# Kernel optimization log

Measured on AMD Instinct MI355X. Metric: run time of the kernel, lower is better.

## Reference

```python
import jax, jax.numpy as jnp
import numpy as np

N_CHARS = 50257
CHAR = 512
HID = 1024
LENGTH = 2048


def setup_inputs() -> dict:
    key = jax.random.key(0)
    ks = jax.random.split(key, 8)
    s = 1.0 / np.sqrt(HID)
    sh = 1.0 / np.sqrt(HID)
    return {
        "inputs": jax.random.normal(ks[0], (HID,), jnp.float32),
        "embed": (jax.random.normal(ks[1], (N_CHARS, CHAR), jnp.float32) * 0.02),
        "W_ih": jax.random.uniform(ks[2], (4 * HID, CHAR), jnp.float32, -s, s),
        "W_hh": jax.random.uniform(ks[3], (4 * HID, HID), jnp.float32, -s, s),
        "b_ih": jax.random.uniform(ks[4], (4 * HID,), jnp.float32, -s, s),
        "b_hh": jax.random.uniform(ks[5], (4 * HID,), jnp.float32, -s, s),
        "W_head": jax.random.uniform(ks[6], (N_CHARS, HID), jnp.float32, -sh, sh),
        "b_head": jax.random.uniform(ks[7], (N_CHARS,), jnp.float32, -sh, sh),
        "length": LENGTH,
        "start": 5,
    }


def _lstm_cell(x, h, c, W_ih, W_hh, b_ih, b_hh):
    # PyTorch gate order: i, f, g, o
    gates = W_ih @ x + b_ih + W_hh @ h + b_hh  # [4H]
    i, f, g, o = jnp.split(gates, 4)
    i = jax.nn.sigmoid(i)
    f = jax.nn.sigmoid(f)
    g = jnp.tanh(g)
    o = jax.nn.sigmoid(o)
    c = f * c + i * g
    h = o * jnp.tanh(c)
    return h, c


def reference(inputs, embed, W_ih, W_hh, b_ih, b_hh, W_head, b_head, length, start):
    h0 = inputs                       # latent used as initial hidden state
    c0 = jnp.zeros_like(inputs)
    x0 = embed[start]                 # [CHAR]

    def step(carry, _):
        h, c, x = carry
        h, c = _lstm_cell(x, h, c, W_ih, W_hh, b_ih, b_hh)
        logits = W_head @ h + b_head  # [N_CHARS]
        char = jnp.argmax(logits)
        x = embed[char]
        return (h, c, x), (char, logits)

    _, (chars, logits) = jax.lax.scan(step, (h0, c0, x0), None, length=length)
    return chars, logits
```

## Files before the change

kernel.cpp:

```cpp
#include <hip/hip_runtime.h>
#include <stdint.h>
#include <math.h>

#define HID   1024
#define CHARD 512
#define NC    50257
#define TLEN  2048
#define NBLK  256
#define NTHR  512
#define NGRP2 2048
#define GR    25
#define GRREG 6
#define GRLDS 19
#define NBH   1571
#define SQ    4064.0f
#define INVSQ (1.0f/4064.0f)
#define QERR  (0.5f/4064.0f)
#define CANDR 192
#define FLAGSTRIDE 16

typedef unsigned long long ull;
typedef unsigned char u8;
typedef float f32x4 __attribute__((ext_vector_type(4)));

__device__ __forceinline__ unsigned ford(float f) {
    unsigned b = __float_as_uint(f);
    return (b & 0x80000000u) ? ~b : (b | 0x80000000u);
}
__device__ __forceinline__ float unford(unsigned u) {
    return __uint_as_float((u & 0x80000000u) ? (u & 0x7FFFFFFFu) : ~u);
}
__device__ __forceinline__ ull packkv(float v, unsigned j) {
    return ((ull)ford(v) << 32) | (ull)(0xFFFFFFFFu - j);
}
__device__ __forceinline__ ull umaxu(ull a, ull b) { return a > b ? a : b; }
__device__ __forceinline__ ull shflx_ull(ull v, int m) {
    unsigned lo = (unsigned)v, hi = (unsigned)(v >> 32);
    lo = __shfl_xor(lo, m);
    hi = __shfl_xor(hi, m);
    return ((ull)hi << 32) | lo;
}

#define ALOADF(p)    __hip_atomic_load((p), __ATOMIC_RELAXED, __HIP_MEMORY_SCOPE_AGENT)
#define ASTORE(p, v) __hip_atomic_store((p), (v), __ATOMIC_RELAXED, __HIP_MEMORY_SCOPE_AGENT)

__global__ __launch_bounds__(256) void k_init(const float* __restrict__ inputs,
                                              float* __restrict__ hh,
                                              float* __restrict__ c,
                                              unsigned* __restrict__ flagarea)
{
    int g = blockIdx.x * 256 + threadIdx.x;
    if (g < HID) { hh[g] = inputs[g]; c[g] = 0.f; }
    for (int i = g; i < 2 * NBLK * FLAGSTRIDE + 16; i += 2048) flagarea[i] = 0u;
}

__global__ __launch_bounds__(256) void k_quant(const float* __restrict__ W,
                                               u8* __restrict__ W8)
{
    size_t base = ((size_t)blockIdx.x * 256 + threadIdx.x) * 16;
    if (base >= (size_t)NC * HID) return;
    const float4* src = (const float4*)(W + base);
    uint out[4];
    #pragma unroll
    for (int g = 0; g < 4; ++g) {
        float4 w = src[g];
        int a0 = (__float2int_rn(w.x * SQ) + 128) & 255;
        int a1 = (__float2int_rn(w.y * SQ) + 128) & 255;
        int a2 = (__float2int_rn(w.z * SQ) + 128) & 255;
        int a3 = (__float2int_rn(w.w * SQ) + 128) & 255;
        out[g] = (uint)(a0 | (a1 << 8) | (a2 << 16) | (a3 << 24));
    }
    *(uint4*)(W8 + base) = make_uint4(out[0], out[1], out[2], out[3]);
}

__device__ __forceinline__ float exact_logit(const float4* hs4,
                                             const float* __restrict__ W_head,
                                             const float* __restrict__ b_head,
                                             int j, int lane)
{
    const float4* wr = (const float4*)(W_head + (size_t)j * HID);
    float a = 0.f;
    #pragma unroll
    for (int m = 0; m < 4; ++m) {
        float4 w = wr[m * 64 + lane], v = hs4[m * 64 + lane];
        a = fmaf(w.x, v.x, a); a = fmaf(w.y, v.y, a);
        a = fmaf(w.z, v.z, a); a = fmaf(w.w, v.w, a);
    }
    #pragma unroll
    for (int off = 32; off > 0; off >>= 1) a += __shfl_xor(a, off);
    return a + b_head[j];
}

__device__ __forceinline__ unsigned resolve_char(const float4* hs4,
                                                 ull* bm, float* abuf,
                                                 const float* __restrict__ W_head,
                                                 const float* __restrict__ b_head,
                                                 float Sh, ull* red8, int tid)
{
    __shared__ int s_cnt, s_gcnt;
    __shared__ int s_grps[32];
    __shared__ int s_rows[CANDR];

    const int wave = tid >> 6;
    const int lane = tid & 63;

    ull bmv[4];
    ull pm = 0ull;
    #pragma unroll
    for (int rep = 0; rep < NGRP2 / NTHR; ++rep) {
        bmv[rep] = ALOADF(&bm[tid + rep * NTHR]);
        pm = umaxu(pm, bmv[rep]);
    }
    #pragma unroll
    for (int off = 32; off > 0; off >>= 1) pm = umaxu(pm, shflx_ull(pm, off));
    if (lane == 0) red8[wave] = pm;
    if (tid == 0) { s_cnt = 0; s_gcnt = 0; }
    __syncthreads();
    pm = red8[0];
    #pragma unroll
    for (int w = 1; w < 8; ++w) pm = umaxu(pm, red8[w]);
    const float mtil = unford((unsigned)(pm >> 32));
    const float E = QERR * Sh * 1.02f + 1e-4f;
    const float thresh = mtil - 2.0f * E;
    const ull pkth = ((ull)ford(thresh)) << 32;

    #pragma unroll
    for (int rep = 0; rep < NGRP2 / NTHR; ++rep) {
        if (bmv[rep] >= pkth) {
            int p = atomicAdd(&s_gcnt, 1);
            if (p < 32) s_grps[p] = tid + rep * NTHR;
        }
    }
    __syncthreads();
    const int ngr = s_gcnt;
    int ncr;
    if (ngr <= 32) {
        for (int gq = 0; gq < ngr; ++gq) {
            const int j = s_grps[gq] * GR + tid;
            if (tid < GR && j < NC) {
                float av = ALOADF(&abuf[j]);
                if (av >= thresh) {
                    int p = atomicAdd(&s_cnt, 1);
                    if (p < CANDR) s_rows[p] = j;
                }
            }
        }
        __syncthreads();
        ncr = s_cnt;
    } else {
        ncr = CANDR + 1;
    }

    ull best = 0ull;
    if (ncr <= CANDR) {
        for (int q = wave; q < ncr; q += 8) {
            const int j = s_rows[q];
            best = umaxu(best, packkv(exact_logit(hs4, W_head, b_head, j, lane),
                                      (unsigned)j));
        }
    } else {
        for (int i = wave; i < NGRP2; i += 8) {
            ull bv = ALOADF(&bm[i]);
            if (bv >= pkth) {
                const int jb = i * GR;
                const int je = jb + GR < NC ? jb + GR : NC;
                for (int j = jb; j < je; ++j) {
                    float av = ALOADF(&abuf[j]);
                    if (av >= thresh)
                        best = umaxu(best, packkv(exact_logit(hs4, W_head, b_head, j, lane),
                                                  (unsigned)j));
                }
            }
        }
    }
    __syncthreads();
    if (lane == 0) red8[wave] = best;
    __syncthreads();
    best = red8[0];
    #pragma unroll
    for (int w = 1; w < 8; ++w) best = umaxu(best, red8[w]);
    unsigned idx = 0xFFFFFFFFu - (unsigned)(best & 0xFFFFFFFFull);
    return idx < NC ? idx : (NC - 1);
}

__device__ __forceinline__ float dot16u(uint4 q, float4 h0, float4 h1,
                                        float4 h2, float4 h3)
{
    float a = 0.f;
    a = fmaf((float)(q.x & 255u), h0.x, a);
    a = fmaf((float)((q.x >> 8) & 255u), h0.y, a);
    a = fmaf((float)((q.x >> 16) & 255u), h0.z, a);
    a = fmaf((float)(q.x >> 24), h0.w, a);
    a = fmaf((float)(q.y & 255u), h1.x, a);
    a = fmaf((float)((q.y >> 8) & 255u), h1.y, a);
    a = fmaf((float)((q.y >> 16) & 255u), h1.z, a);
    a = fmaf((float)(q.y >> 24), h1.w, a);
    a = fmaf((float)(q.z & 255u), h2.x, a);
    a = fmaf((float)((q.z >> 8) & 255u), h2.y, a);
    a = fmaf((float)((q.z >> 16) & 255u), h2.z, a);
    a = fmaf((float)(q.z >> 24), h2.w, a);
    a = fmaf((float)(q.w & 255u), h3.x, a);
    a = fmaf((float)((q.w >> 8) & 255u), h3.y, a);
    a = fmaf((float)((q.w >> 16) & 255u), h3.z, a);
    a = fmaf((float)(q.w >> 24), h3.w, a);
    return a;
}

__global__ __launch_bounds__(NTHR, 1) void k_persist(
    const float* __restrict__ W_ih, const float* __restrict__ W_hh,
    const float* __restrict__ b_ih, const float* __restrict__ b_hh,
    const float* __restrict__ embed,
    const float* __restrict__ W_head, const float* __restrict__ b_head,
    const u8* __restrict__ W8,
    float* hh, float* abuf, ull* bm,
    float* __restrict__ chars_out, const int* __restrict__ startp,
    unsigned* flags, unsigned* gen)
{
    __shared__ uint4  w8L[8][GRLDS][64];
    __shared__ float4 hs4[HID / 4];
    __shared__ float4 xs4[CHARD / 4];
    __shared__ ull    red8[8];
    __shared__ float  sred[8], sred2[8];
    __shared__ int    s_brk;

    const int b    = blockIdx.x;
    const int tid  = threadIdx.x;
    const int wave = tid >> 6;
    const int lane = tid & 63;
    const int rL   = b * 4 + wave;
    const int g    = b * 8 + wave;
    const int jb   = g * GR;
    const u8* Wp   = W8 + (size_t)jb * HID;

    uint4 qb[GRREG];
    #pragma unroll
    for (int rr = 0; rr < GRREG; ++rr) {
        const int j = jb + rr;
        qb[rr] = (j < NC) ? ((const uint4*)(Wp + (size_t)rr * HID))[lane]
                          : make_uint4(0, 0, 0, 0);
    }
    #pragma unroll
    for (int rr = 0; rr < GRLDS; ++rr) {
        const int j = jb + GRREG + rr;
        w8L[wave][rr][lane] = (j < NC)
            ? ((const uint4*)(Wp + (size_t)(GRREG + rr) * HID))[lane]
            : make_uint4(0, 0, 0, 0);
    }

    float bsum[4] = {0.f, 0.f, 0.f, 0.f};
    if (wave < 4) {
        #pragma unroll
        for (int q = 0; q < 4; ++q) bsum[q] = b_ih[q * HID + rL] + b_hh[q * HID + rL];
    }
    if (tid == 0) s_brk = 0;
    float creg = 0.f;
    __syncthreads();

    float Sh;
    {
        float sa = 0.f;
        if (tid < 256) {
            float4 hv = ((const float4*)hh)[tid];
            hs4[tid] = hv;
            sa = fabsf(hv.x) + fabsf(hv.y) + fabsf(hv.z) + fabsf(hv.w);
        }
        #pragma unroll
        for (int off = 32; off > 0; off >>= 1) sa += __shfl_xor(sa, off);
        if (lane == 0) sred[wave] = sa;
        __syncthreads();
        Sh = 0.f;
        #pragma unroll
        for (int w = 0; w < 8; ++w) Sh += sred[w];
    }

    unsigned bk = 0;

    #define GRIDBAR()                                                              \
    do {                                                                           \
        ++bk;                                                                      \
        __syncthreads();                                                           \
        if (b == 0) {                                                              \
            if (!s_brk && tid > 0 && tid < NBLK) {                                 \
                int guard = 0;                                                     \
                while (__hip_atomic_load(&flags[tid * FLAGSTRIDE],                 \
                         __ATOMIC_RELAXED, __HIP_MEMORY_SCOPE_AGENT) < bk) {       \
                    __builtin_amdgcn_s_sleep(1);                                   \
                    if (++guard > (1 << 24)) { s_brk = 1; break; }                 \
                }                                                                  \
            }                                                                      \
            __syncthreads();                                                       \
            if (tid < NBLK)                                                        \
                __hip_atomic_store(&gen[tid * FLAGSTRIDE], bk, __ATOMIC_RELAXED,   \
                                   __HIP_MEMORY_SCOPE_AGENT);                      \
        } else {                                                                   \
            if (tid == 0) {                                                        \
                __hip_atomic_store(&flags[b * FLAGSTRIDE], bk, __ATOMIC_RELAXED,   \
                                   __HIP_MEMORY_SCOPE_AGENT);                      \
                if (!s_brk) {                                                      \
                    int guard = 0;                                                 \
                    while (__hip_atomic_load(&gen[b * FLAGSTRIDE],                 \
                             __ATOMIC_RELAXED, __HIP_MEMORY_SCOPE_AGENT) < bk) {   \
                        __builtin_amdgcn_s_sleep(1);                               \
                        if (++guard > (1 << 24)) { s_brk = 1; break; }             \
                    }                                                              \
                }                                                                  \
            }                                                                      \
            __syncthreads();                                                       \
        }                                                                          \
    } while (0)

    for (int t = 0; t < TLEN; ++t) {
        unsigned idx;
        if (t == 0) {
            idx = (unsigned)startp[0];
        } else {
            idx = resolve_char(hs4, bm, abuf, W_head, b_head, Sh, red8, tid);
            if (b == 0 && tid == 0) chars_out[t - 1] = (float)idx;
        }
        if (tid < 128) xs4[tid] = ((const float4*)(embed + (size_t)idx * CHARD))[tid];
        __syncthreads();

        if (wave < 4) {
            float acc[4];
            #pragma unroll
            for (int q = 0; q < 4; ++q) {
                const float4* wi = (const float4*)(W_ih + (size_t)(q * HID + rL) * CHARD);
                const float4* wh = (const float4*)(W_hh + (size_t)(q * HID + rL) * HID);
                float a = 0.f;
                #pragma unroll
                for (int m = 0; m < 2; ++m) {
                    float4 w = wi[m * 64 + lane], v = xs4[m * 64 + lane];
                    a = fmaf(w.x, v.x, a); a = fmaf(w.y, v.y, a);
                    a = fmaf(w.z, v.z, a); a = fmaf(w.w, v.w, a);
                }
                #pragma unroll
                for (int m = 0; m < 4; ++m) {
                    float4 w = wh[m * 64 + lane], v = hs4[m * 64 + lane];
                    a = fmaf(w.x, v.x, a); a = fmaf(w.y, v.y, a);
                    a = fmaf(w.z, v.z, a); a = fmaf(w.w, v.w, a);
                }
                acc[q] = a;
            }
            #pragma unroll
            for (int q = 0; q < 4; ++q) {
                #pragma unroll
                for (int off = 32; off > 0; off >>= 1) acc[q] += __shfl_xor(acc[q], off);
            }
            if (lane == 0) {
                float ig = 1.f / (1.f + expf(-(acc[0] + bsum[0])));
                float fg = 1.f / (1.f + expf(-(acc[1] + bsum[1])));
                float gg = tanhf(acc[2] + bsum[2]);
                float og = 1.f / (1.f + expf(-(acc[3] + bsum[3])));
                creg = fg * creg + ig * gg;
                ASTORE(&hh[(size_t)(t + 1) * HID + rL], og * tanhf(creg));
            }
        }

        GRIDBAR();

        {
            float sa = 0.f, ss = 0.f;
            if (tid < 256) {
                float4 hv = ((const float4*)(hh + (size_t)(t + 1) * HID))[tid];
                hs4[tid] = hv;
                sa = fabsf(hv.x) + fabsf(hv.y) + fabsf(hv.z) + fabsf(hv.w);
                ss = hv.x + hv.y + hv.z + hv.w;
            }
            #pragma unroll
            for (int off = 32; off > 0; off >>= 1) {
                sa += __shfl_xor(sa, off);
                ss += __shfl_xor(ss, off);
            }
            if (lane == 0) { sred[wave] = sa; sred2[wave] = ss; }
        }
        __syncthreads();
        float Hsum = 0.f;
        Sh = 0.f;
        #pragma unroll
        for (int w = 0; w < 8; ++w) { Sh += sred[w]; Hsum += sred2[w]; }

        const float4 H0 = hs4[lane * 4 + 0];
        const float4 H1 = hs4[lane * 4 + 1];
        const float4 H2 = hs4[lane * 4 + 2];
        const float4 H3 = hs4[lane * 4 + 3];

        ull pmw = 0ull;
        #pragma unroll
        for (int rr = 0; rr < GRREG; ++rr) {
            const int j = jb + rr;
            if (j < NC) {
                float a = dot16u(qb[rr], H0, H1, H2, H3);
                #pragma unroll
                for (int off = 32; off > 0; off >>= 1) a += __shfl_xor(a, off);
                const float v = (a - 128.f * Hsum) * INVSQ + b_head[j];
                if (lane == 0) ASTORE(&abuf[j], v);
                pmw = umaxu(pmw, packkv(v, (unsigned)j));
            }
        }
        #pragma unroll
        for (int rr = 0; rr < GRLDS; ++rr) {
            const int j = jb + GRREG + rr;
            if (j < NC) {
                float a = dot16u(w8L[wave][rr][lane], H0, H1, H2, H3);
                #pragma unroll
                for (int off = 32; off > 0; off >>= 1) a += __shfl_xor(a, off);
                const float v = (a - 128.f * Hsum) * INVSQ + b_head[j];
                if (lane == 0) ASTORE(&abuf[j], v);
                pmw = umaxu(pmw, packkv(v, (unsigned)j));
            }
        }
        if (lane == 0) ASTORE(&bm[g], pmw);

        GRIDBAR();
    }

    if (b == 0) {
        unsigned idx = resolve_char(hs4, bm, abuf, W_head, b_head, Sh, red8, tid);
        if (tid == 0) chars_out[TLEN - 1] = (float)idx;
    }
    #undef GRIDBAR
}

#define GJ 64
#define GT 128
#define GK 16
__global__ __launch_bounds__(256) void k_gemm(const float* __restrict__ W_head,
                                              const float* __restrict__ b_head,
                                              const float* __restrict__ hh,
                                              float* __restrict__ logits)
{
    __shared__ float Ws[GK][GJ + 4];
    __shared__ float Hs[GK][GT + 1];

    const int tid = threadIdx.x;
    const int j0 = blockIdx.x * GJ;
    const int t0 = blockIdx.y * GT;
    const int tj = tid & 15;
    const int tt = tid >> 4;

    const int wlj = tid >> 2;
    const int wlk = (tid & 3) * 4;
    const int hlt = tid >> 1;
    const int hlk = (tid & 1) * 8;
    const float* Wrow = W_head + (size_t)(j0 + wlj) * HID;
    const bool wvalid = (j0 + wlj) < NC;

    float acc[8][4];
    #pragma unroll
    for (int bb = 0; bb < 8; ++bb)
        #pragma unroll
        for (int a = 0; a < 4; ++a) acc[bb][a] = 0.f;

    for (int k0 = 0; k0 < HID; k0 += GK) {
        __syncthreads();
        float4 wv = wvalid ? *(const float4*)(Wrow + k0 + wlk) : make_float4(0, 0, 0, 0);
        Ws[wlk + 0][wlj] = wv.x; Ws[wlk + 1][wlj] = wv.y;
        Ws[wlk + 2][wlj] = wv.z; Ws[wlk + 3][wlj] = wv.w;
        const float* hp = hh + (size_t)(t0 + hlt + 1) * HID + k0 + hlk;
        float4 a0 = *(const float4*)hp;
        float4 a1 = *(const float4*)(hp + 4);
        Hs[hlk + 0][hlt] = a0.x; Hs[hlk + 1][hlt] = a0.y;
        Hs[hlk + 2][hlt] = a0.z; Hs[hlk + 3][hlt] = a0.w;
        Hs[hlk + 4][hlt] = a1.x; Hs[hlk + 5][hlt] = a1.y;
        Hs[hlk + 6][hlt] = a1.z; Hs[hlk + 7][hlt] = a1.w;
        __syncthreads();
        #pragma unroll
        for (int kk = 0; kk < GK; ++kk) {
            float4 w4 = *(const float4*)&Ws[kk][tj * 4];
            float hvv[8];
            #pragma unroll
            for (int bb = 0; bb < 8; ++bb) hvv[bb] = Hs[kk][tt + 16 * bb];
            #pragma unroll
            for (int bb = 0; bb < 8; ++bb) {
                acc[bb][0] = fmaf(w4.x, hvv[bb], acc[bb][0]);
                acc[bb][1] = fmaf(w4.y, hvv[bb], acc[bb][1]);
                acc[bb][2] = fmaf(w4.z, hvv[bb], acc[bb][2]);
                acc[bb][3] = fmaf(w4.w, hvv[bb], acc[bb][3]);
            }
        }
    }

    const int j = j0 + tj * 4;
    float b0 = (j + 0 < NC) ? b_head[j + 0] : 0.f;
    float b1 = (j + 1 < NC) ? b_head[j + 1] : 0.f;
    float b2 = (j + 2 < NC) ? b_head[j + 2] : 0.f;
    float b3 = (j + 3 < NC) ? b_head[j + 3] : 0.f;
    #pragma unroll
    for (int bb = 0; bb < 8; ++bb) {
        const int t = t0 + tt + 16 * bb;
        float* dst = logits + (size_t)t * NC + j;
        if (j + 3 < NC) {
            f32x4 o = { acc[bb][0] + b0, acc[bb][1] + b1,
                        acc[bb][2] + b2, acc[bb][3] + b3 };
            __builtin_nontemporal_store(o, (f32x4*)dst);
        } else {
            if (j + 0 < NC) dst[0] = acc[bb][0] + b0;
            if (j + 1 < NC) dst[1] = acc[bb][1] + b1;
            if (j + 2 < NC) dst[2] = acc[bb][2] + b2;
        }
    }
}

__global__ __launch_bounds__(256) void k_init_fb(const float* __restrict__ inputs,
                                                 const int* __restrict__ startp,
                                                 float* __restrict__ h0,
                                                 float* __restrict__ c,
                                                 ull* __restrict__ blockmax)
{
    int tid = blockIdx.x * 256 + threadIdx.x;
    if (tid < NBH) blockmax[tid] = (tid == 0) ? packkv(3.0e38f, (unsigned)startp[0]) : 0ull;
    if (tid < HID) { h0[tid] = inputs[tid]; c[tid] = 0.f; }
}

__global__ __launch_bounds__(256) void k_lstm_fb(const float* __restrict__ W_ih,
                                                 const float* __restrict__ W_hh,
                                                 const float* __restrict__ b_ih,
                                                 const float* __restrict__ b_hh,
                                                 const float* __restrict__ embed,
                                                 const ull* __restrict__ blockmax,
                                                 const float* __restrict__ h_in,
                                                 float* __restrict__ h_out,
                                                 float* __restrict__ c,
                                                 float* __restrict__ chars_out,
                                                 int t)
{
    __shared__ float4 xs4[CHARD / 4];
    __shared__ float4 hs4[HID / 4];
    __shared__ ull    red[256];
    const int tid = threadIdx.x;
    ull pm = 0ull;
    for (int i = tid; i < NBH; i += 256) pm = umaxu(pm, blockmax[i]);
    red[tid] = pm;
    __syncthreads();
    for (int s = 128; s > 0; s >>= 1) {
        if (tid < s) red[tid] = umaxu(red[tid], red[tid + s]);
        __syncthreads();
    }
    const unsigned idx = 0xFFFFFFFFu - (unsigned)(red[0] & 0xFFFFFFFFull);
    if (t > 0 && blockIdx.x == 0 && tid == 0) chars_out[t - 1] = (float)idx;
    const float4* ex = (const float4*)(embed + (size_t)idx * CHARD);
    if (tid < 128) xs4[tid] = ex[tid];
    hs4[tid] = ((const float4*)h_in)[tid];
    __syncthreads();
    const int wave = tid >> 6, lane = tid & 63;
    const int r = blockIdx.x * 4 + wave;
    float acc[4];
    #pragma unroll
    for (int q = 0; q < 4; ++q) {
        const float4* wi = (const float4*)(W_ih + (size_t)(q * HID + r) * CHARD);
        const float4* wh = (const float4*)(W_hh + (size_t)(q * HID + r) * HID);
        float a = 0.f;
        #pragma unroll
        for (int m = 0; m < 2; ++m) {
            float4 w = wi[m * 64 + lane], v = xs4[m * 64 + lane];
            a = fmaf(w.x, v.x, a); a = fmaf(w.y, v.y, a);
            a = fmaf(w.z, v.z, a); a = fmaf(w.w, v.w, a);
        }
        #pragma unroll
        for (int m = 0; m < 4; ++m) {
            float4 w = wh[m * 64 + lane], v = hs4[m * 64 + lane];
            a = fmaf(w.x, v.x, a); a = fmaf(w.y, v.y, a);
            a = fmaf(w.z, v.z, a); a = fmaf(w.w, v.w, a);
        }
        acc[q] = a;
    }
    #pragma unroll
    for (int q = 0; q < 4; ++q)
        #pragma unroll
        for (int off = 32; off > 0; off >>= 1) acc[q] += __shfl_xor(acc[q], off);
    if (lane == 0) {
        float zi = acc[0] + b_ih[r]           + b_hh[r];
        float zf = acc[1] + b_ih[HID + r]     + b_hh[HID + r];
        float zg = acc[2] + b_ih[2 * HID + r] + b_hh[2 * HID + r];
        float zo = acc[3] + b_ih[3 * HID + r] + b_hh[3 * HID + r];
        float ig = 1.f / (1.f + expf(-zi));
        float fg = 1.f / (1.f + expf(-zf));
        float gg = tanhf(zg);
        float og = 1.f / (1.f + expf(-zo));
        float cn = fg * c[r] + ig * gg;
        c[r] = cn;
        h_out[r] = og * tanhf(cn);
    }
}

__global__ __launch_bounds__(256) void k_head_fb(const float* __restrict__ W_head,
                                                 const float* __restrict__ b_head,
                                                 const float* __restrict__ h_in,
                                                 float* __restrict__ logits,
                                                 ull* __restrict__ blockmax)
{
    __shared__ float4 hs4[HID / 4];
    __shared__ ull    wmax[4];
    const int tid = threadIdx.x;
    hs4[tid] = ((const float4*)h_in)[tid];
    __syncthreads();
    const int wave = tid >> 6, lane = tid & 63;
    const int base = blockIdx.x * 32 + wave * 8;
    ull pm = 0ull;
    #pragma unroll
    for (int rep = 0; rep < 8; ++rep) {
        const int j = base + rep;
        if (j < NC) {
            const float4* w = (const float4*)(W_head + (size_t)j * HID);
            float a = 0.f;
            #pragma unroll
            for (int m = 0; m < 4; ++m) {
                float4 ww = w[m * 64 + lane], v = hs4[m * 64 + lane];
                a = fmaf(ww.x, v.x, a); a = fmaf(ww.y, v.y, a);
                a = fmaf(ww.z, v.z, a); a = fmaf(ww.w, v.w, a);
            }
            #pragma unroll
            for (int off = 32; off > 0; off >>= 1) a += __shfl_xor(a, off);
            const float v = a + b_head[j];
            if (lane == 0) __builtin_nontemporal_store(v, &logits[j]);
            pm = umaxu(pm, packkv(v, (unsigned)j));
        }
    }
    if (lane == 0) wmax[wave] = pm;
    __syncthreads();
    if (tid == 0)
        blockmax[blockIdx.x] = umaxu(umaxu(wmax[0], wmax[1]), umaxu(wmax[2], wmax[3]));
}

__global__ __launch_bounds__(256) void k_final_fb(const ull* __restrict__ blockmax,
                                                  float* __restrict__ chars_out)
{
    __shared__ ull red[256];
    const int tid = threadIdx.x;
    ull pm = 0ull;
    for (int i = tid; i < NBH; i += 256) pm = umaxu(pm, blockmax[i]);
    red[tid] = pm;
    __syncthreads();
    for (int s = 128; s > 0; s >>= 1) {
        if (tid < s) red[tid] = umaxu(red[tid], red[tid + s]);
        __syncthreads();
    }
    if (tid == 0)
        chars_out[TLEN - 1] = (float)(0xFFFFFFFFu - (unsigned)(red[0] & 0xFFFFFFFFull));
}

extern "C" void kernel_launch(void* const* d_in, const int* in_sizes, int n_in,
                              void* d_out, int out_size, void* d_ws, size_t ws_size,
                              hipStream_t stream)
{
    const float* inputs = (const float*)d_in[0];
    const float* embed  = (const float*)d_in[1];
    const float* W_ih   = (const float*)d_in[2];
    const float* W_hh   = (const float*)d_in[3];
    const float* b_ih   = (const float*)d_in[4];
    const float* b_hh   = (const float*)d_in[5];
    const float* W_head = (const float*)d_in[6];
    const float* b_head = (const float*)d_in[7];
    const int*   startp = (const int*)d_in[9];

    float* out        = (float*)d_out;
    float* chars_out  = out;
    float* logits_out = out + TLEN;

    char* ws = (char*)d_ws;
    const size_t off_hh    = 0;
    const size_t off_c     = off_hh + (size_t)(TLEN + 1) * HID * 4;
    const size_t off_ab    = off_c + (size_t)HID * 4;
    const size_t off_bm    = (off_ab + (size_t)NC * 4 + 15) & ~(size_t)15;
    const size_t off_flags = (off_bm + (size_t)NGRP2 * 8 + 63) & ~(size_t)63;
    const size_t off_w8    = (off_flags + (size_t)(2 * NBLK * FLAGSTRIDE + 16) * 4 + 15)
                             & ~(size_t)15;
    const size_t need      = off_w8 + (size_t)NC * HID;

    if (ws_size >= need) {
        float*    hh    = (float*)(ws + off_hh);
        float*    c     = (float*)(ws + off_c);
        float*    abuf  = (float*)(ws + off_ab);
        ull*      bm    = (ull*)(ws + off_bm);
        unsigned* flags = (unsigned*)(ws + off_flags);
        unsigned* gen   = flags + NBLK * FLAGSTRIDE;
        u8*       W8    = (u8*)(ws + off_w8);

        hipLaunchKernelGGL(k_init, dim3(8), dim3(256), 0, stream, inputs, hh, c, flags);
        hipLaunchKernelGGL(k_quant, dim3((NC * HID / 16 + 255) / 256), dim3(256), 0,
                           stream, W_head, W8);
        hipLaunchKernelGGL(k_persist, dim3(NBLK), dim3(NTHR), 0, stream,
                           W_ih, W_hh, b_ih, b_hh, embed, W_head, b_head, W8,
                           hh, abuf, bm, chars_out, startp, flags, gen);
        hipLaunchKernelGGL(k_gemm, dim3((NC + GJ - 1) / GJ, TLEN / GT), dim3(256), 0,
                           stream, W_head, b_head, hh, logits_out);
    } else {
        float* h0 = (float*)(ws);
        float* h1 = (float*)(ws + 4096);
        float* c  = (float*)(ws + 8192);
        ull* blockmax = (ull*)(ws + 12288);
        hipLaunchKernelGGL(k_init_fb, dim3(7), dim3(256), 0, stream,
                           inputs, startp, h0, c, blockmax);
        for (int t = 0; t < TLEN; ++t) {
            const float* hin = (t & 1) ? h1 : h0;
            float*       hout = (t & 1) ? h0 : h1;
            hipLaunchKernelGGL(k_lstm_fb, dim3(256), dim3(256), 0, stream,
                               W_ih, W_hh, b_ih, b_hh, embed, blockmax,
                               hin, hout, c, chars_out, t);
            hipLaunchKernelGGL(k_head_fb, dim3(NBH), dim3(256), 0, stream,
                               W_head, b_head, hout,
                               logits_out + (size_t)t * NC, blockmax);
        }
        hipLaunchKernelGGL(k_final_fb, dim3(1), dim3(256), 0, stream, blockmax, chars_out);
    }
}
```

Baseline: 46.54 ms.

## Pack approximate head maxima into generation-tagged 32-bit words and prune stores

Replaces the 64-bit per-group max keys and per-row float logit buffer with 32-bit words that hold a ceiling-rounded 16-bit ordered value and a 16-bit step tag. Only rows near their group's top are written, with one coalesced store per wave instead of a lane-0 store per row. Candidate scanning is spread across waves, and the fallback path uses a ballot. The goal is less global traffic and fewer serialized stores in the per-step argmax, at the cost of coarser thresholds that may admit more candidates for exact recomputation.

```diff
diff --git a/kernel.cpp b/kernel.cpp
--- a/kernel.cpp
+++ b/kernel.cpp
@@ -33,6 +33,10 @@
 __device__ __forceinline__ ull packkv(float v, unsigned j) {
     return ((ull)ford(v) << 32) | (ull)(0xFFFFFFFFu - j);
 }
+__device__ __forceinline__ unsigned ceil16(float v) {
+    unsigned u = ford(v);
+    return (u >> 16) + ((u & 0xFFFFu) ? 1u : 0u);
+}
 __device__ __forceinline__ ull umaxu(ull a, ull b) { return a > b ? a : b; }
 __device__ __forceinline__ ull shflx_ull(ull v, int m) {
     unsigned lo = (unsigned)v, hi = (unsigned)(v >> 32);
@@ -47,11 +51,15 @@
 __global__ __launch_bounds__(256) void k_init(const float* __restrict__ inputs,
                                               float* __restrict__ hh,
                                               float* __restrict__ c,
-                                              unsigned* __restrict__ flagarea)
+                                              unsigned* __restrict__ flagarea,
+                                              unsigned* __restrict__ bm4,
+                                              unsigned* __restrict__ abuf16)
 {
     int g = blockIdx.x * 256 + threadIdx.x;
     if (g < HID) { hh[g] = inputs[g]; c[g] = 0.f; }
-    for (int i = g; i < 2 * NBLK * FLAGSTRIDE + 16; i += 2048) flagarea[i] = 0u;
+    for (int i = g; i < 2 * NBLK * FLAGSTRIDE; i += 2048) flagarea[i] = 0u;
+    if (g < NGRP2) bm4[g] = 0u;
+    for (int i = g; i < NC; i += 2048) abuf16[i] = 0u;
 }
 
 __global__ __launch_bounds__(256) void k_quant(const float* __restrict__ W,
@@ -91,65 +99,75 @@
     return a + b_head[j];
 }
 
-__device__ __forceinline__ unsigned resolve_char(const float4* hs4,
-                                                 ull* bm, float* abuf,
-                                                 const float* __restrict__ W_head,
-                                                 const float* __restrict__ b_head,
-                                                 float Sh, ull* red8, int tid)
+__device__ unsigned resolve_slim(const float4* hs4,
+                                 const unsigned* bm4, const unsigned* abuf16,
+                                 const float* __restrict__ W_head,
+                                 const float* __restrict__ b_head,
+                                 float Sh, unsigned gen16, int tid)
 {
     __shared__ int s_cnt, s_gcnt;
     __shared__ int s_grps[32];
     __shared__ int s_rows[CANDR];
+    __shared__ unsigned mred[8];
+    __shared__ ull red8[8];
 
     const int wave = tid >> 6;
     const int lane = tid & 63;
 
-    ull bmv[4];
-    ull pm = 0ull;
-    #pragma unroll
-    for (int rep = 0; rep < NGRP2 / NTHR; ++rep) {
-        bmv[rep] = ALOADF(&bm[tid + rep * NTHR]);
-        pm = umaxu(pm, bmv[rep]);
-    }
-    #pragma unroll
-    for (int off = 32; off > 0; off >>= 1) pm = umaxu(pm, shflx_ull(pm, off));
-    if (lane == 0) red8[wave] = pm;
+    unsigned bv[4];
+    unsigned m16 = 0u;
+    #pragma unroll
+    for (int k = 0; k < 4; ++k) {
+        bv[k] = ALOADF(&bm4[tid * 4 + k]);
+        if ((bv[k] & 0xFFFFu) == gen16) {
+            unsigned v = bv[k] >> 16;
+            if (v > m16) m16 = v;
+        }
+    }
     if (tid == 0) { s_cnt = 0; s_gcnt = 0; }
-    __syncthreads();
-    pm = red8[0];
-    #pragma unroll
-    for (int w = 1; w < 8; ++w) pm = umaxu(pm, red8[w]);
-    const float mtil = unford((unsigned)(pm >> 32));
+    #pragma unroll
+    for (int off = 32; off > 0; off >>= 1) {
+        unsigned o = __shfl_xor(m16, off);
+        if (o > m16) m16 = o;
+    }
+    if (lane == 0) mred[wave] = m16;
+    __syncthreads();
+    m16 = mred[0];
+    #pragma unroll
+    for (int w = 1; w < 8; ++w) if (mred[w] > m16) m16 = mred[w];
+
+    const float mtil_f = unford((m16 > 0 ? m16 - 1 : 0) << 16);
     const float E = QERR * Sh * 1.02f + 1e-4f;
-    const float thresh = mtil - 2.0f * E;
-    const ull pkth = ((ull)ford(thresh)) << 32;
-
-    #pragma unroll
-    for (int rep = 0; rep < NGRP2 / NTHR; ++rep) {
-        if (bmv[rep] >= pkth) {
+    const float thresh = mtil_f - 2.0f * E;
+    const unsigned th16 = ford(thresh) >> 16;
+
+    #pragma unroll
+    for (int k = 0; k < 4; ++k) {
+        unsigned v = bv[k];
+        if ((v & 0xFFFFu) == gen16 && (v >> 16) >= th16) {
             int p = atomicAdd(&s_gcnt, 1);
-            if (p < 32) s_grps[p] = tid + rep * NTHR;
+            if (p < 32) s_grps[p] = tid * 4 + k;
         }
     }
     __syncthreads();
     const int ngr = s_gcnt;
     int ncr;
     if (ngr <= 32) {
-        for (int gq = 0; gq < ngr; ++gq) {
-            const int j = s_grps[gq] * GR + tid;
-            if (tid < GR && j < NC) {
-                float av = ALOADF(&abuf[j]);
-                if (av >= thresh) {
-                    int p = atomicAdd(&s_cnt, 1);
-                    if (p < CANDR) s_rows[p] = j;
+        for (int gq = wave; gq < ngr; gq += 8) {
+            if (lane < GR) {
+                const int j = s_grps[gq] * GR + lane;
+                if (j < NC) {
+                    unsigned a = ALOADF(&abuf16[j]);
+                    if ((a & 0xFFFFu) == gen16 && (a >> 16) >= th16) {
+                        int p = atomicAdd(&s_cnt, 1);
+                        if (p < CANDR) s_rows[p] = j;
+                    }
                 }
             }
         }
         __syncthreads();
         ncr = s_cnt;
-    } else {
-        ncr = CANDR + 1;
-    }
+    } else ncr = CANDR + 1;
 
     ull best = 0ull;
     if (ncr <= CANDR) {
@@ -160,15 +178,21 @@
         }
     } else {
         for (int i = wave; i < NGRP2; i += 8) {
-            ull bv = ALOADF(&bm[i]);
-            if (bv >= pkth) {
-                const int jb = i * GR;
-                const int je = jb + GR < NC ? jb + GR : NC;
-                for (int j = jb; j < je; ++j) {
-                    float av = ALOADF(&abuf[j]);
-                    if (av >= thresh)
-                        best = umaxu(best, packkv(exact_logit(hs4, W_head, b_head, j, lane),
-                                                  (unsigned)j));
+            unsigned v = ALOADF(&bm4[i]);
+            if ((v & 0xFFFFu) == gen16 && (v >> 16) >= th16) {
+                const int j0 = i * GR;
+                bool c = false;
+                if (lane < GR && j0 + lane < NC) {
+                    unsigned a = ALOADF(&abuf16[j0 + lane]);
+                    c = ((a & 0xFFFFu) == gen16 && (a >> 16) >= th16);
+                }
+                ull cnd = __ballot(c);
+                while (cnd) {
+                    const int s = __builtin_ctzll(cnd);
+                    cnd &= cnd - 1;
+                    const int j = j0 + s;
+                    best = umaxu(best, packkv(exact_logit(hs4, W_head, b_head, j, lane),
+                                              (unsigned)j));
                 }
             }
         }
@@ -212,16 +236,14 @@
     const float* __restrict__ embed,
     const float* __restrict__ W_head, const float* __restrict__ b_head,
     const u8* __restrict__ W8,
-    float* hh, float* abuf, ull* bm,
+    float* hh, unsigned* abuf16, unsigned* bm4,
     float* __restrict__ chars_out, const int* __restrict__ startp,
     unsigned* flags, unsigned* gen)
 {
     __shared__ uint4  w8L[8][GRLDS][64];
     __shared__ float4 hs4[HID / 4];
     __shared__ float4 xs4[CHARD / 4];
-    __shared__ ull    red8[8];
     __shared__ float  sred[8], sred2[8];
-    __shared__ int    s_brk;
 
     const int b    = blockIdx.x;
     const int tid  = threadIdx.x;
@@ -252,7 +274,6 @@
         #pragma unroll
         for (int q = 0; q < 4; ++q) bsum[q] = b_ih[q * HID + rL] + b_hh[q * HID + rL];
     }
-    if (tid == 0) s_brk = 0;
     float creg = 0.f;
     __syncthreads();
 
@@ -280,29 +301,23 @@
         ++bk;                                                                      \
         __syncthreads();                                                           \
         if (b == 0) {                                                              \
-            if (!s_brk && tid > 0 && tid < NBLK) {                                 \
+            if (tid > 0 && tid < NBLK) {                                           \
                 int guard = 0;                                                     \
-                while (__hip_atomic_load(&flags[tid * FLAGSTRIDE],                 \
-                         __ATOMIC_RELAXED, __HIP_MEMORY_SCOPE_AGENT) < bk) {       \
+                while (ALOADF(&flags[tid * FLAGSTRIDE]) < bk) {                    \
                     __builtin_amdgcn_s_sleep(1);                                   \
-                    if (++guard > (1 << 24)) { s_brk = 1; break; }                 \
+                    if (++guard > (1 << 24)) break;                                \
                 }                                                                  \
             }                                                                      \
             __syncthreads();                                                       \
             if (tid < NBLK)                                                        \
-                __hip_atomic_store(&gen[tid * FLAGSTRIDE], bk, __ATOMIC_RELAXED,   \
-                                   __HIP_MEMORY_SCOPE_AGENT);                      \
+                ASTORE(&gen[tid * FLAGSTRIDE], bk);                                \
         } else {                                                                   \
             if (tid == 0) {                                                        \
-                __hip_atomic_store(&flags[b * FLAGSTRIDE], bk, __ATOMIC_RELAXED,   \
-                                   __HIP_MEMORY_SCOPE_AGENT);                      \
-                if (!s_brk) {                                                      \
-                    int guard = 0;                                                 \
-                    while (__hip_atomic_load(&gen[b * FLAGSTRIDE],                 \
-                             __ATOMIC_RELAXED, __HIP_MEMORY_SCOPE_AGENT) < bk) {   \
-                        __builtin_amdgcn_s_sleep(1);                               \
-                        if (++guard > (1 << 24)) { s_brk = 1; break; }             \
-                    }                                                              \
+                ASTORE(&flags[b * FLAGSTRIDE], bk);                                \
+                int guard = 0;                                                     \
+                while (ALOADF(&gen[b * FLAGSTRIDE]) < bk) {                        \
+                    __builtin_amdgcn_s_sleep(1);                                   \
+                    if (++guard > (1 << 24)) break;                                \
                 }                                                                  \
             }                                                                      \
             __syncthreads();                                                       \
@@ -314,7 +329,8 @@
         if (t == 0) {
             idx = (unsigned)startp[0];
         } else {
-            idx = resolve_char(hs4, bm, abuf, W_head, b_head, Sh, red8, tid);
+            idx = resolve_slim(hs4, bm4, abuf16, W_head, b_head, Sh,
+                               (unsigned)t & 0xFFFFu, tid);
             if (b == 0 && tid == 0) chars_out[t - 1] = (float)idx;
         }
         if (tid < 128) xs4[tid] = ((const float4*)(embed + (size_t)idx * CHARD))[tid];
@@ -383,39 +399,49 @@
         const float4 H1 = hs4[lane * 4 + 1];
         const float4 H2 = hs4[lane * 4 + 2];
         const float4 H3 = hs4[lane * 4 + 3];
-
-        ull pmw = 0ull;
-        #pragma unroll
-        for (int rr = 0; rr < GRREG; ++rr) {
-            const int j = jb + rr;
-            if (j < NC) {
-                float a = dot16u(qb[rr], H0, H1, H2, H3);
-                #pragma unroll
-                for (int off = 32; off > 0; off >>= 1) a += __shfl_xor(a, off);
-                const float v = (a - 128.f * Hsum) * INVSQ + b_head[j];
-                if (lane == 0) ASTORE(&abuf[j], v);
-                pmw = umaxu(pmw, packkv(v, (unsigned)j));
-            }
-        }
-        #pragma unroll
-        for (int rr = 0; rr < GRLDS; ++rr) {
-            const int j = jb + GRREG + rr;
-            if (j < NC) {
-                float a = dot16u(w8L[wave][rr][lane], H0, H1, H2, H3);
-                #pragma unroll
-                for (int off = 32; off > 0; off >>= 1) a += __shfl_xor(a, off);
-                const float v = (a - 128.f * Hsum) * INVSQ + b_head[j];
-                if (lane == 0) ASTORE(&abuf[j], v);
-                pmw = umaxu(pmw, packkv(v, (unsigned)j));
-            }
-        }
-        if (lane == 0) ASTORE(&bm[g], pmw);
+        const unsigned genN = (unsigned)(t + 1) & 0xFFFFu;
+
+        if (jb < NC) {
+            ull pmw = 0ull;
+            float sv = -3.0e38f;
+            #pragma unroll
+            for (int rr = 0; rr < GRREG; ++rr) {
+                const int j = jb + rr;
+                if (j < NC) {
+                    float a = dot16u(qb[rr], H0, H1, H2, H3);
+                    #pragma unroll
+                    for (int off = 32; off > 0; off >>= 1) a += __shfl_xor(a, off);
+                    const float v = (a - 128.f * Hsum) * INVSQ + b_head[j];
+                    if (lane == rr) sv = v;
+                    pmw = umaxu(pmw, packkv(v, (unsigned)j));
+                }
+            }
+            #pragma unroll
+            for (int rr = 0; rr < GRLDS; ++rr) {
+                const int j = jb + GRREG + rr;
+                if (j < NC) {
+                    float a = dot16u(w8L[wave][rr][lane], H0, H1, H2, H3);
+                    #pragma unroll
+                    for (int off = 32; off > 0; off >>= 1) a += __shfl_xor(a, off);
+                    const float v = (a - 128.f * Hsum) * INVSQ + b_head[j];
+                    if (lane == GRREG + rr) sv = v;
+                    pmw = umaxu(pmw, packkv(v, (unsigned)j));
+                }
+            }
+            const float gtop = unford((unsigned)(pmw >> 32));
+            const float E2 = QERR * Sh * 1.02f + 1e-4f;
+            if (lane < GR && (jb + lane) < NC && sv >= gtop - 2.0f * E2)
+                ASTORE(&abuf16[jb + lane], (ceil16(sv) << 16) | genN);
+            if (lane == 0)
+                ASTORE(&bm4[g], (ceil16(gtop) << 16) | genN);
+        }
 
         GRIDBAR();
     }
 
     if (b == 0) {
-        unsigned idx = resolve_char(hs4, bm, abuf, W_head, b_head, Sh, red8, tid);
+        unsigned idx = resolve_slim(hs4, bm4, abuf16, W_head, b_head, Sh,
+                                    (unsigned)TLEN & 0xFFFFu, tid);
         if (tid == 0) chars_out[TLEN - 1] = (float)idx;
     }
     #undef GRIDBAR
@@ -658,30 +684,31 @@
     float* logits_out = out + TLEN;
 
     char* ws = (char*)d_ws;
-    const size_t off_hh    = 0;
-    const size_t off_c     = off_hh + (size_t)(TLEN + 1) * HID * 4;
-    const size_t off_ab    = off_c + (size_t)HID * 4;
-    const size_t off_bm    = (off_ab + (size_t)NC * 4 + 15) & ~(size_t)15;
-    const size_t off_flags = (off_bm + (size_t)NGRP2 * 8 + 63) & ~(size_t)63;
-    const size_t off_w8    = (off_flags + (size_t)(2 * NBLK * FLAGSTRIDE + 16) * 4 + 15)
-                             & ~(size_t)15;
-    const size_t need      = off_w8 + (size_t)NC * HID;
+    const size_t off_hh  = 0;
+    const size_t off_c   = off_hh + (size_t)(TLEN + 1) * HID * 4;
+    const size_t off_ab  = (off_c + (size_t)HID * 4 + 15) & ~(size_t)15;
+    const size_t off_bm  = (off_ab + (size_t)NC * 4 + 15) & ~(size_t)15;
+    const size_t off_fl  = (off_bm + (size_t)NGRP2 * 4 + 63) & ~(size_t)63;
+    const size_t off_w8  = (off_fl + (size_t)(2 * NBLK * FLAGSTRIDE) * 4 + 15)
+                           & ~(size_t)15;
+    const size_t need    = off_w8 + (size_t)NC * HID;
 
     if (ws_size >= need) {
-        float*    hh    = (float*)(ws + off_hh);
-        float*    c     = (float*)(ws + off_c);
-        float*    abuf  = (float*)(ws + off_ab);
-        ull*      bm    = (ull*)(ws + off_bm);
-        unsigned* flags = (unsigned*)(ws + off_flags);
-        unsigned* gen   = flags + NBLK * FLAGSTRIDE;
-        u8*       W8    = (u8*)(ws + off_w8);
-
-        hipLaunchKernelGGL(k_init, dim3(8), dim3(256), 0, stream, inputs, hh, c, flags);
+        float*    hh     = (float*)(ws + off_hh);
+        float*    c      = (float*)(ws + off_c);
+        unsigned* abuf16 = (unsigned*)(ws + off_ab);
+        unsigned* bm4    = (unsigned*)(ws + off_bm);
+        unsigned* flags  = (unsigned*)(ws + off_fl);
+        unsigned* gen    = flags + NBLK * FLAGSTRIDE;
+        u8*       W8     = (u8*)(ws + off_w8);
+
+        hipLaunchKernelGGL(k_init, dim3(8), dim3(256), 0, stream,
+                           inputs, hh, c, flags, bm4, abuf16);
         hipLaunchKernelGGL(k_quant, dim3((NC * HID / 16 + 255) / 256), dim3(256), 0,
                            stream, W_head, W8);
         hipLaunchKernelGGL(k_persist, dim3(NBLK), dim3(NTHR), 0, stream,
                            W_ih, W_hh, b_ih, b_hh, embed, W_head, b_head, W8,
-                           hh, abuf, bm, chars_out, startp, flags, gen);
+                           hh, abuf16, bm4, chars_out, startp, flags, gen);
         hipLaunchKernelGGL(k_gemm, dim3((NC + GJ - 1) / GJ, TLEN / GT), dim3(256), 0,
                            stream, W_head, b_head, hh, logits_out);
     } else {
```

Result: faster. 45.43 ms, median of 2 (-2.4%).
